# Kernel optimization log

Hardware: AMD Instinct MI355X
Metric: run time of the kernel (lower is better)

## Reference

```python
import jax, jax.numpy as jnp
import numpy as np

B, T, C, H = 4, 4096, 1024, 64


def setup_inputs() -> dict:
    key = jax.random.key(0)
    ks = jax.random.split(key, 7)
    s = C ** -0.5
    return {
        "x": jax.random.normal(ks[0], (B, T, C), dtype=jnp.float32),
        "Wk": jax.random.normal(ks[1], (C, H), dtype=jnp.float32) * s,
        "bk": jax.random.normal(ks[2], (H,), dtype=jnp.float32) * 0.02,
        "Wq": jax.random.normal(ks[3], (C, H), dtype=jnp.float32) * s,
        "bq": jax.random.normal(ks[4], (H,), dtype=jnp.float32) * 0.02,
        "Wv": jax.random.normal(ks[5], (C, H), dtype=jnp.float32) * s,
        "bv": jax.random.normal(ks[6], (H,), dtype=jnp.float32) * 0.02,
    }


def reference(x, Wk, bk, Wq, bq, Wv, bv):
    Bx, Tx, Cx = x.shape
    k = x @ Wk + bk            # [B,T,H]
    q = x @ Wq + bq            # [B,T,H]
    v = x @ Wv + bv            # [B,T,H]
    scale = Cx ** -0.5         # NOTE: source scales by n_embed^-0.5, not head_size
    # Faithful to source: scores = K @ Q^T (rows indexed by key position)
    wei = jnp.einsum("bth,bsh->bts", k, q) * scale  # [B,T,T]
    causal = jnp.tril(jnp.ones((Tx, Tx), dtype=bool))
    wei = jnp.where(causal, wei, -jnp.inf)
    wei = jax.nn.softmax(wei, axis=-1)
    out = jnp.einsum("bts,bsh->bth", wei, v)        # [B,T,H]
    return out
```

## Files before the change

### kernel.cpp

```cpp
#include <hip/hip_runtime.h>
#include <hip/hip_bf16.h>
#include <math.h>


typedef __attribute__((ext_vector_type(8))) short bf16x8;
typedef __attribute__((ext_vector_type(4))) short bf16x4;
typedef __attribute__((ext_vector_type(4))) float f32x4;

#define MFMA16(a, b, c) __builtin_amdgcn_mfma_f32_16x16x32_bf16(a, b, c, 0, 0, 0)

__device__ __forceinline__ short f2bf(float f) {
    __hip_bfloat16 h = __float2bfloat16(f);
    return *reinterpret_cast<short*>(&h);
}

#if __has_builtin(__builtin_amdgcn_exp2f)
__device__ __forceinline__ float fexp2(float x) { return __builtin_amdgcn_exp2f(x); }
#else
__device__ __forceinline__ float fexp2(float x) { return exp2f(x); }
#endif

static constexpr int T = 4096;
static constexpr int C = 1024;
static constexpr int H = 64;
static constexpr int BATCH = 4;
static constexpr int M = BATCH * T;
static constexpr int CPB = 288;
static constexpr float LOG2E = 1.44269504088896340736f;
static constexpr float KSCALE = 0.03125f * LOG2E;


__global__ __launch_bounds__(256) void wtrans_kernel(
    const float* __restrict__ Wk, const float* __restrict__ Wq,
    const float* __restrict__ Wv, short* __restrict__ Wt_g)
{
    const int blk = blockIdx.x;
    const int tid = threadIdx.x;
    __shared__ short Wl[64][72];
    const int mat = blk / 16, k0 = (blk % 16) * 64;
    const float* W = (mat == 0) ? Wk : (mat == 1) ? Wq : Wv;
    const int hr = (tid & 15) * 4, kr = tid >> 4;
    #pragma unroll
    for (int pass = 0; pass < 4; ++pass) {
        int k = kr + pass * 16;
        float4 v = *(const float4*)&W[(size_t)(k0 + k) * H + hr];
        Wl[hr + 0][k] = f2bf(v.x);
        Wl[hr + 1][k] = f2bf(v.y);
        Wl[hr + 2][k] = f2bf(v.z);
        Wl[hr + 3][k] = f2bf(v.w);
    }
    __syncthreads();
    const int h = tid >> 2, kk = (tid & 3) * 16;
    bf16x8 o0 = *(const bf16x8*)&Wl[h][kk];
    bf16x8 o1 = *(const bf16x8*)&Wl[h][kk + 8];
    *(bf16x8*)&Wt_g[(size_t)(mat * 64 + h) * C + k0 + kk] = o0;
    *(bf16x8*)&Wt_g[(size_t)(mat * 64 + h) * C + k0 + kk + 8] = o1;
}

__global__ __launch_bounds__(256) void proj_kernel(
    const float* __restrict__ x, const short* __restrict__ Wt_g,
    const float* __restrict__ bk, const float* __restrict__ bq,
    const float* __restrict__ bv,
    short* __restrict__ Kf, short* __restrict__ Qf, short* __restrict__ Vf)
{
    __shared__ short As[2][32][72];
    __shared__ short Ws[2][192][72];
    const int tid = threadIdx.x;
    const int wv = tid >> 6, lane = tid & 63, quad = lane >> 4, l16 = lane & 15;
    const int grp = wv >> 1, w2 = wv & 1;
    const int m0 = blockIdx.x * 32;
    const int arow = tid >> 3, ac8 = (tid & 7) * 8;

    f32x4 acc[6];
    #pragma unroll
    for (int i = 0; i < 6; ++i)
        for (int j = 0; j < 4; ++j) acc[i][j] = 0.f;

    float4 xa0, xa1;
    bf16x8 wl[6];
    auto gload = [&](int k0) {
        xa0 = *(const float4*)&x[(size_t)(m0 + arow) * C + k0 + ac8];
        xa1 = *(const float4*)&x[(size_t)(m0 + arow) * C + k0 + ac8 + 4];
        #pragma unroll
        for (int i = 0; i < 6; ++i) {
            int idx = tid + i * 256;
            wl[i] = *(const bf16x8*)&Wt_g[(size_t)(idx >> 3) * C + k0 + (idx & 7) * 8];
        }
    };
    auto lwrite = [&](int p) {
        bf16x8 av;
        av[0] = f2bf(xa0.x); av[1] = f2bf(xa0.y); av[2] = f2bf(xa0.z); av[3] = f2bf(xa0.w);
        av[4] = f2bf(xa1.x); av[5] = f2bf(xa1.y); av[6] = f2bf(xa1.z); av[7] = f2bf(xa1.w);
        *(bf16x8*)&As[p][arow][ac8] = av;
        #pragma unroll
        for (int i = 0; i < 6; ++i) {
            int idx = tid + i * 256;
            *(bf16x8*)&Ws[p][idx >> 3][(idx & 7) * 8] = wl[i];
        }
    };

    gload(0);
    lwrite(0);
    __syncthreads();
    for (int it = 0; it < 16; ++it) {
        const int p = it & 1;
        if (it < 15) gload((it + 1) * 64);
        bf16x8 a0 = *(const bf16x8*)&As[p][w2 * 16 + l16][quad * 8];
        bf16x8 a1 = *(const bf16x8*)&As[p][w2 * 16 + l16][32 + quad * 8];
        #pragma unroll
        for (int tn = 0; tn < 6; ++tn) {
            bf16x8 b0 = *(const bf16x8*)&Ws[p][grp * 96 + tn * 16 + l16][quad * 8];
            bf16x8 b1 = *(const bf16x8*)&Ws[p][grp * 96 + tn * 16 + l16][32 + quad * 8];
            acc[tn] = MFMA16(a0, b0, acc[tn]);
            acc[tn] = MFMA16(a1, b1, acc[tn]);
        }
        if (it < 15) {
            lwrite((it + 1) & 1);
            __syncthreads();
        }
    }
    const int tile = blockIdx.x >> 1, bh = blockIdx.x & 1;
    short* stage = &Ws[0][0][0];
    #pragma unroll
    for (int tn = 0; tn < 6; ++tn) {
        int gc = grp * 96 + tn * 16 + l16;
        int mat = gc >> 6, h = gc & 63;
        const float* bias = (mat == 0) ? bk : (mat == 1) ? bq : bv;
        float bb = bias[h];
        float sc = (mat == 0) ? KSCALE : 1.f;
        #pragma unroll
        for (int r = 0; r < 4; ++r) {
            int s = w2 * 16 + quad * 4 + r;
            short val = f2bf((acc[tn][r] + bb) * sc);
            int o;
            if (mat == 2) {
                o = 4096 + (h >> 4) * 512 + (((s >> 3) * 16) + (h & 15)) * 8 + (s & 7);
            } else {
                o = mat * 2048 + (s >> 4) * 1024 + (h >> 5) * 512
                    + ((((h & 31) >> 3) * 16) + (s & 15)) * 8 + (h & 7);
            }
            stage[o] = val;
        }
    }
    __syncthreads();
    {
        int voff = tid * 8;
        *(bf16x8*)&Kf[(size_t)tile * 4096 + bh * 2048 + voff] =
            *(const bf16x8*)&stage[voff];
        *(bf16x8*)&Qf[(size_t)tile * 4096 + bh * 2048 + voff] =
            *(const bf16x8*)&stage[2048 + voff];
        int hn = tid >> 6, u = voff & 511;
        *(bf16x8*)&Vf[(size_t)tile * 4096 + hn * 1024 + bh * 512 + u] =
            *(const bf16x8*)&stage[4096 + voff];
    }
}

__global__ __launch_bounds__(256) void attn_part_kernel(
    const short* __restrict__ Kf, const short* __restrict__ Qf,
    const short* __restrict__ Vf, float* __restrict__ Pb,
    float* __restrict__ lnPb)
{
    __shared__ short Pl[4][2][16][76];
    __shared__ float Ob[64][68];
    __shared__ float lnb[64];
    const int tid = threadIdx.x;
    const int wv = tid >> 6, lane = tid & 63;
    const int quad = lane >> 4, l16 = lane & 15;
    const int sp = wv & 1, sh = wv >> 1;
    const int g = blockIdx.x;
    const int x = g & 7;
    const int i = g >> 3;
    const int b = x >> 1;
    int tt, chi;
    if ((x & 1) == 0) {
        if (i < 64)       { chi = 0; tt = i; }
        else if (i < 120) { chi = 1; tt = 8 + (i - 64); }
        else if (i < 136) { chi = 6; tt = 48 + (i - 120); }
        else              { chi = 7; tt = 56 + (i - 136); }
    } else {
        if (i < 48)       { chi = 2; tt = 16 + i; }
        else if (i < 88)  { chi = 3; tt = 24 + (i - 48); }
        else if (i < 120) { chi = 4; tt = 32 + (i - 88); }
        else              { chi = 5; tt = 40 + (i - 120); }
    }
    const int kch = tt / 8 + 1;
    const int c = 4 * kch * (kch - 1) + (tt - 8 * (kch - 1)) * kch + chi;
    const int sA = sp * 2, sB = sp * 2 + 1;
    const int st0 = chi * 8;
    const int st1 = min(st0 + 8, tt + 1);

    const short* kt = Kf + (size_t)(b * 64 + tt) * 4096 + lane * 8;
    bf16x8 kf0a = *(const bf16x8*)(kt + sA * 1024);
    bf16x8 kf1a = *(const bf16x8*)(kt + sA * 1024 + 512);
    bf16x8 kf0b = *(const bf16x8*)(kt + sB * 1024);
    bf16x8 kf1b = *(const bf16x8*)(kt + sB * 1024 + 512);

    bf16x8 ones;
    #pragma unroll
    for (int j = 0; j < 8; ++j) ones[j] = (short)0x3F80;

    f32x4 oA[4], oB[4], lnA, lnB;
    #pragma unroll
    for (int i2 = 0; i2 < 4; ++i2)
        for (int j = 0; j < 4; ++j) { oA[i2][j] = 0.f; oB[i2][j] = 0.f; }
    #pragma unroll
    for (int j = 0; j < 4; ++j) { lnA[j] = 0.f; lnB[j] = 0.f; }

    const int myb = st0 + sh;
    const short* qp = Qf + (size_t)(b * 64 + myb) * 4096 + lane * 8;
    const short* vp = Vf + (size_t)(b * 64 + myb) * 4096 + lane * 8;

    bf16x8 qc0[4], qc1[4];
    f32x4 sAc[4], sBc[4];
    if (myb < st1) {
        #pragma unroll
        for (int tn = 0; tn < 4; ++tn) {
            qc0[tn] = *(const bf16x8*)(qp + tn * 1024);
            qc1[tn] = *(const bf16x8*)(qp + tn * 1024 + 512);
        }
        __builtin_amdgcn_s_setprio(1);
        #pragma unroll
        for (int tn = 0; tn < 4; ++tn) {
            #pragma unroll
            for (int j = 0; j < 4; ++j) { sAc[tn][j] = 0.f; sBc[tn][j] = 0.f; }
            sAc[tn] = MFMA16(qc0[tn], kf0a, sAc[tn]);
            sAc[tn] = MFMA16(qc1[tn], kf1a, sAc[tn]);
            sBc[tn] = MFMA16(qc0[tn], kf0b, sBc[tn]);
            sBc[tn] = MFMA16(qc1[tn], kf1b, sBc[tn]);
        }
        __builtin_amdgcn_s_setprio(0);
    }

    for (int st = myb; st < st1; st += 2) {
        bf16x8 vb0[4], vb1[4];
        #pragma unroll
        for (int hn = 0; hn < 4; ++hn) {
            vb0[hn] = *(const bf16x8*)(vp + hn * 1024);
            vb1[hn] = *(const bf16x8*)(vp + hn * 1024 + 512);
        }
        const size_t qoff = (st + 2 < st1) ? 8192 : 0;
        #pragma unroll
        for (int tn = 0; tn < 4; ++tn) {
            qc0[tn] = *(const bf16x8*)(qp + qoff + tn * 1024);
            qc1[tn] = *(const bf16x8*)(qp + qoff + tn * 1024 + 512);
        }
        const bool diag = (st == tt);
        #pragma unroll
        for (int tn = 0; tn < 4; ++tn) {
            bf16x4 pa, pb;
            #pragma unroll
            for (int r = 0; r < 4; ++r) {
                float va = sAc[tn][r], vb = sBc[tn][r];
                if (diag) {
                    int scol = tn * 16 + quad * 4 + r;
                    if (scol > sA * 16 + l16) va = -INFINITY;
                    if (scol > sB * 16 + l16) vb = -INFINITY;
                }
                pa[r] = f2bf(fexp2(va));
                pb[r] = f2bf(fexp2(vb));
            }
            *(bf16x4*)&Pl[wv][0][l16][tn * 16 + quad * 4] = pa;
            *(bf16x4*)&Pl[wv][1][l16][tn * 16 + quad * 4] = pb;
        }
        bf16x8 aA0 = *(const bf16x8*)&Pl[wv][0][l16][quad * 8];
        bf16x8 aA1 = *(const bf16x8*)&Pl[wv][0][l16][32 + quad * 8];
        bf16x8 aB0 = *(const bf16x8*)&Pl[wv][1][l16][quad * 8];
        bf16x8 aB1 = *(const bf16x8*)&Pl[wv][1][l16][32 + quad * 8];
        if (st + 2 < st1) {
            __builtin_amdgcn_s_setprio(1);
            #pragma unroll
            for (int tn = 0; tn < 4; ++tn) {
                #pragma unroll
                for (int j = 0; j < 4; ++j) { sAc[tn][j] = 0.f; sBc[tn][j] = 0.f; }
                sAc[tn] = MFMA16(qc0[tn], kf0a, sAc[tn]);
                sAc[tn] = MFMA16(qc1[tn], kf1a, sAc[tn]);
                sBc[tn] = MFMA16(qc0[tn], kf0b, sBc[tn]);
                sBc[tn] = MFMA16(qc1[tn], kf1b, sBc[tn]);
            }
            __builtin_amdgcn_s_setprio(0);
        }
        __builtin_amdgcn_s_setprio(1);
        #pragma unroll
        for (int hn = 0; hn < 4; ++hn) {
            oA[hn] = MFMA16(aA0, vb0[hn], oA[hn]);
            oA[hn] = MFMA16(aA1, vb1[hn], oA[hn]);
            oB[hn] = MFMA16(aB0, vb0[hn], oB[hn]);
            oB[hn] = MFMA16(aB1, vb1[hn], oB[hn]);
        }
        lnA = MFMA16(aA0, ones, lnA);
        lnA = MFMA16(aA1, ones, lnA);
        lnB = MFMA16(aB0, ones, lnB);
        lnB = MFMA16(aB1, ones, lnB);
        __builtin_amdgcn_s_setprio(0);
        qp += 8192;
        vp += 8192;
    }

    const int rbase = sp * 32;
    if (sh == 1) {
        #pragma unroll
        for (int hn = 0; hn < 4; ++hn)
            #pragma unroll
            for (int r = 0; r < 4; ++r) {
                Ob[rbase + quad * 4 + r][hn * 16 + l16] = oA[hn][r];
                Ob[rbase + 16 + quad * 4 + r][hn * 16 + l16] = oB[hn][r];
            }
        if (l16 == 0) {
            #pragma unroll
            for (int r = 0; r < 4; ++r) {
                lnb[rbase + quad * 4 + r] = lnA[r];
                lnb[rbase + 16 + quad * 4 + r] = lnB[r];
            }
        }
    }
    __syncthreads();
    if (sh == 0) {
        #pragma unroll
        for (int hn = 0; hn < 4; ++hn)
            #pragma unroll
            for (int r = 0; r < 4; ++r) {
                int ra = rbase + quad * 4 + r;
                int rb = ra + 16;
                Ob[ra][hn * 16 + l16] += oA[hn][r];
                Ob[rb][hn * 16 + l16] += oB[hn][r];
            }
        if (l16 == 0) {
            float* lc = lnPb + (size_t)(b * CPB + c) * 64;
            #pragma unroll
            for (int r = 0; r < 4; ++r) {
                lc[rbase + quad * 4 + r] = lnA[r] + lnb[rbase + quad * 4 + r];
                lc[rbase + 16 + quad * 4 + r] = lnB[r] + lnb[rbase + 16 + quad * 4 + r];
            }
        }
    }
    __syncthreads();
    float4* Pc4 = (float4*)(Pb + (size_t)(b * CPB + c) * 4096);
    #pragma unroll
    for (int i2 = 0; i2 < 4; ++i2) {
        int idx = tid + i2 * 256;
        int row = idx >> 4, c4 = (idx & 15) * 4;
        Pc4[idx] = *(const float4*)&Ob[row][c4];
    }
}

__global__ __launch_bounds__(256) void reduce_norm_kernel(
    const float* __restrict__ Pb, const float* __restrict__ lnPb,
    float* __restrict__ out)
{
    const int blk = blockIdx.x;
    const int b = blk >> 6, tt = blk & 63;
    const int k = tt / 8 + 1;
    const int base_c = 4 * k * (k - 1) + (tt - 8 * (k - 1)) * k;
    const int tid = threadIdx.x;
    __shared__ float lnS[64];
    if (tid < 64) {
        float s = 0.f;
        for (int i = 0; i < k; ++i)
            s += lnPb[(size_t)(b * CPB + base_c + i) * 64 + tid];
        lnS[tid] = 1.f / s;
    }
    __syncthreads();
    float4 acc[4];
    #pragma unroll
    for (int j = 0; j < 4; ++j) acc[j] = {0.f, 0.f, 0.f, 0.f};
    for (int i = 0; i < k; ++i) {
        const float4* p4 = (const float4*)(Pb + (size_t)(b * CPB + base_c + i) * 4096);
        #pragma unroll
        for (int j = 0; j < 4; ++j) {
            float4 v = p4[tid + j * 256];
            acc[j].x += v.x; acc[j].y += v.y; acc[j].z += v.z; acc[j].w += v.w;
        }
    }
    float4* o4 = (float4*)out;
    const size_t obase = ((size_t)b * T + (size_t)tt * 64) * 16;
    #pragma unroll
    for (int j = 0; j < 4; ++j) {
        int idx = tid + j * 256;
        float inv = lnS[idx >> 4];
        float4 v = acc[j];
        v.x *= inv; v.y *= inv; v.z *= inv; v.w *= inv;
        o4[obase + idx] = v;
    }
}

extern "C" void kernel_launch(void* const* d_in, const int* in_sizes, int n_in,
                              void* d_out, int out_size, void* d_ws, size_t ws_size,
                              hipStream_t stream) {
    const float* x  = (const float*)d_in[0];
    const float* Wk = (const float*)d_in[1];
    const float* bk = (const float*)d_in[2];
    const float* Wq = (const float*)d_in[3];
    const float* bq = (const float*)d_in[4];
    const float* Wv = (const float*)d_in[5];
    const float* bv = (const float*)d_in[6];
    float* out = (float*)d_out;

    char* ws = (char*)d_ws;
    size_t off = 0;
    short* Kf   = (short*)(ws + off); off += (size_t)M * H * 2;
    short* Qf   = (short*)(ws + off); off += (size_t)M * H * 2;
    short* Vf   = (short*)(ws + off); off += (size_t)M * H * 2;
    short* Wt_g = (short*)(ws + off); off += (size_t)192 * C * 2;
    float* Pb   = (float*)(ws + off); off += (size_t)BATCH * CPB * 4096 * 4;
    float* lnPb = (float*)(ws + off); off += (size_t)BATCH * CPB * 64 * 4;

    wtrans_kernel<<<48, 256, 0, stream>>>(Wk, Wq, Wv, Wt_g);
    proj_kernel<<<M / 32, 256, 0, stream>>>(x, Wt_g, bk, bq, bv, Kf, Qf, Vf);
    attn_part_kernel<<<BATCH * CPB, 256, 0, stream>>>(Kf, Qf, Vf, Pb, lnPb);
    reduce_norm_kernel<<<BATCH * 64, 256, 0, stream>>>(Pb, lnPb, out);
}
```

Baseline: 146.4 us.

## Write single-chunk tiles directly to output and store partials in fp16

Query tiles covered by a single key chunk (kch==1) now normalize and write their result straight to the output inside the attention kernel. The reduce kernel is launched only for the remaining multi-chunk tiles. The partial output buffer is stored as fp16 instead of fp32, halving partial write and read traffic. This trades some precision in the unnormalized partial sums, and fp16 could overflow if a partial is large.

```diff
diff --git a/kernel.cpp b/kernel.cpp
--- a/kernel.cpp
+++ b/kernel.cpp
@@ -1,11 +1,14 @@
 #include <hip/hip_runtime.h>
 #include <hip/hip_bf16.h>
+#include <hip/hip_fp16.h>
 #include <math.h>
 
 
 typedef __attribute__((ext_vector_type(8))) short bf16x8;
 typedef __attribute__((ext_vector_type(4))) short bf16x4;
 typedef __attribute__((ext_vector_type(4))) float f32x4;
+typedef __attribute__((ext_vector_type(8))) _Float16 halfx8;
+typedef __attribute__((ext_vector_type(4))) _Float16 halfx4;
 
 #define MFMA16(a, b, c) __builtin_amdgcn_mfma_f32_16x16x32_bf16(a, b, c, 0, 0, 0)
 
@@ -157,8 +160,8 @@
 
 __global__ __launch_bounds__(256) void attn_part_kernel(
     const short* __restrict__ Kf, const short* __restrict__ Qf,
-    const short* __restrict__ Vf, float* __restrict__ Pb,
-    float* __restrict__ lnPb)
+    const short* __restrict__ Vf, _Float16* __restrict__ Pb,
+    float* __restrict__ lnPb, float* __restrict__ out)
 {
     __shared__ short Pl[4][2][16][76];
     __shared__ float Ob[64][68];
@@ -325,30 +328,53 @@
                 Ob[rb][hn * 16 + l16] += oB[hn][r];
             }
         if (l16 == 0) {
-            float* lc = lnPb + (size_t)(b * CPB + c) * 64;
             #pragma unroll
             for (int r = 0; r < 4; ++r) {
-                lc[rbase + quad * 4 + r] = lnA[r] + lnb[rbase + quad * 4 + r];
-                lc[rbase + 16 + quad * 4 + r] = lnB[r] + lnb[rbase + 16 + quad * 4 + r];
-            }
-        }
-    }
-    __syncthreads();
-    float4* Pc4 = (float4*)(Pb + (size_t)(b * CPB + c) * 4096);
-    #pragma unroll
-    for (int i2 = 0; i2 < 4; ++i2) {
-        int idx = tid + i2 * 256;
-        int row = idx >> 4, c4 = (idx & 15) * 4;
-        Pc4[idx] = *(const float4*)&Ob[row][c4];
+                float mA = lnA[r] + lnb[rbase + quad * 4 + r];
+                float mB = lnB[r] + lnb[rbase + 16 + quad * 4 + r];
+                if (kch == 1) {
+                    lnb[rbase + quad * 4 + r] = mA;
+                    lnb[rbase + 16 + quad * 4 + r] = mB;
+                } else {
+                    float* lc = lnPb + (size_t)(b * CPB + c) * 64;
+                    lc[rbase + quad * 4 + r] = mA;
+                    lc[rbase + 16 + quad * 4 + r] = mB;
+                }
+            }
+        }
+    }
+    __syncthreads();
+    if (kch == 1) {
+        float* ob = out + (size_t)(b * T + tt * 64) * H;
+        #pragma unroll
+        for (int i2 = 0; i2 < 4; ++i2) {
+            int idx = tid + i2 * 256;
+            int row = idx >> 4, c4 = (idx & 15) * 4;
+            float inv = 1.f / lnb[row];
+            float4 v = *(const float4*)&Ob[row][c4];
+            v.x *= inv; v.y *= inv; v.z *= inv; v.w *= inv;
+            *(float4*)&ob[row * H + c4] = v;
+        }
+    } else {
+        _Float16* Pc = Pb + (size_t)(b * CPB + c) * 4096;
+        #pragma unroll
+        for (int i2 = 0; i2 < 2; ++i2) {
+            int idx = tid + i2 * 256;
+            int row = idx >> 3, c8 = (idx & 7) * 8;
+            halfx8 hv;
+            #pragma unroll
+            for (int j = 0; j < 8; ++j) hv[j] = (_Float16)Ob[row][c8 + j];
+            *(halfx8*)&Pc[idx * 8] = hv;
+        }
     }
 }
 
 __global__ __launch_bounds__(256) void reduce_norm_kernel(
-    const float* __restrict__ Pb, const float* __restrict__ lnPb,
+    const _Float16* __restrict__ Pb, const float* __restrict__ lnPb,
     float* __restrict__ out)
 {
     const int blk = blockIdx.x;
-    const int b = blk >> 6, tt = blk & 63;
+    const int b = blk / 56, tt = 8 + blk % 56;
     const int k = tt / 8 + 1;
     const int base_c = 4 * k * (k - 1) + (tt - 8 * (k - 1)) * k;
     const int tid = threadIdx.x;
@@ -364,11 +390,12 @@
     #pragma unroll
     for (int j = 0; j < 4; ++j) acc[j] = {0.f, 0.f, 0.f, 0.f};
     for (int i = 0; i < k; ++i) {
-        const float4* p4 = (const float4*)(Pb + (size_t)(b * CPB + base_c + i) * 4096);
+        const _Float16* p = Pb + (size_t)(b * CPB + base_c + i) * 4096;
         #pragma unroll
         for (int j = 0; j < 4; ++j) {
-            float4 v = p4[tid + j * 256];
-            acc[j].x += v.x; acc[j].y += v.y; acc[j].z += v.z; acc[j].w += v.w;
+            halfx4 hv = *(const halfx4*)&p[(tid + j * 256) * 4];
+            acc[j].x += (float)hv[0]; acc[j].y += (float)hv[1];
+            acc[j].z += (float)hv[2]; acc[j].w += (float)hv[3];
         }
     }
     float4* o4 = (float4*)out;
@@ -397,15 +424,15 @@
 
     char* ws = (char*)d_ws;
     size_t off = 0;
-    short* Kf   = (short*)(ws + off); off += (size_t)M * H * 2;
-    short* Qf   = (short*)(ws + off); off += (size_t)M * H * 2;
-    short* Vf   = (short*)(ws + off); off += (size_t)M * H * 2;
-    short* Wt_g = (short*)(ws + off); off += (size_t)192 * C * 2;
-    float* Pb   = (float*)(ws + off); off += (size_t)BATCH * CPB * 4096 * 4;
-    float* lnPb = (float*)(ws + off); off += (size_t)BATCH * CPB * 64 * 4;
+    short* Kf      = (short*)(ws + off);    off += (size_t)M * H * 2;
+    short* Qf      = (short*)(ws + off);    off += (size_t)M * H * 2;
+    short* Vf      = (short*)(ws + off);    off += (size_t)M * H * 2;
+    short* Wt_g    = (short*)(ws + off);    off += (size_t)192 * C * 2;
+    _Float16* Pb   = (_Float16*)(ws + off); off += (size_t)BATCH * CPB * 4096 * 2;
+    float* lnPb    = (float*)(ws + off);    off += (size_t)BATCH * CPB * 64 * 4;
 
     wtrans_kernel<<<48, 256, 0, stream>>>(Wk, Wq, Wv, Wt_g);
     proj_kernel<<<M / 32, 256, 0, stream>>>(x, Wt_g, bk, bq, bv, Kf, Qf, Vf);
-    attn_part_kernel<<<BATCH * CPB, 256, 0, stream>>>(Kf, Qf, Vf, Pb, lnPb);
-    reduce_norm_kernel<<<BATCH * 64, 256, 0, stream>>>(Pb, lnPb, out);
-}
+    attn_part_kernel<<<BATCH * CPB, 256, 0, stream>>>(Kf, Qf, Vf, Pb, lnPb, out);
+    reduce_norm_kernel<<<BATCH * 56, 256, 0, stream>>>(Pb, lnPb, out);
+}
```

Result: no change. 147.7 us (+0.9%).
